# Kernel tuning notes

Hardware: AMD Instinct MI355X
Metric: run time of the kernel (lower is better)

Reference implementation:

```python
import jax, jax.numpy as jnp
import numpy as np

B, S, D, H = 2, 2048, 512, 8
HID = 512
DH = HID // H  # 64


def setup_inputs() -> dict:
    key = jax.random.key(0)
    ks = jax.random.split(key, 11)
    sc = 0.02
    return {
        "q": jax.random.normal(ks[0], (B, S, D), jnp.float32),
        "k": jax.random.normal(ks[1], (B, S, D), jnp.float32),
        "v": jax.random.normal(ks[2], (B, S, D), jnp.float32),
        "Wq": jax.random.normal(ks[3], (D, HID), jnp.float32) * sc,
        "bq": jnp.zeros((HID,), jnp.float32),
        "Wk": jax.random.normal(ks[4], (D, HID), jnp.float32) * sc,
        "bk": jnp.zeros((HID,), jnp.float32),
        "Wv": jax.random.normal(ks[5], (D, HID), jnp.float32) * sc,
        "bv": jnp.zeros((HID,), jnp.float32),
        "Wo": jax.random.normal(ks[6], (HID, D), jnp.float32) * sc,
        "bo": jnp.zeros((D,), jnp.float32),
    }


def reference(q, k, v, Wq, bq, Wk, bk, Wv, bv, Wo, bo):
    # Linear projections: [B,S,D] -> [B,S,HID]
    qp = q @ Wq + bq
    kp = k @ Wk + bk
    vp = v @ Wv + bv
    # Faithful to torch .view(B, -1, S, head_dim): raw reshape, NOT a
    # [B,S,H,d] transpose. Head i reads a contiguous block of the buffer.
    qh = qp.reshape(B, H, S, DH)
    kh = kp.reshape(B, H, S, DH)
    vh = vp.reshape(B, H, S, DH)
    # scores [B,H,S,S]; NOTE: original divides by sqrt(d) AFTER softmax.
    scores = jnp.einsum("bhsd,bhtd->bhst", qh, kh)
    attn = jax.nn.softmax(scores, axis=-1) / np.sqrt(DH).astype(np.float32)
    ctx = jnp.einsum("bhst,bhtd->bhsd", attn, vh)
    # torch.cat over heads along last dim -> [B,S,H*d] with head blocks
    concat = jnp.transpose(ctx, (0, 2, 1, 3)).reshape(B, S, HID)
    return concat @ Wo + bo
```

## Files before the change

### kernel.cpp

```cpp
#include <hip/hip_runtime.h>
#include <hip/hip_bf16.h>

typedef __bf16 bf16_t;
typedef __bf16 bf16x8 __attribute__((ext_vector_type(8)));
typedef __bf16 bf16x4 __attribute__((ext_vector_type(4)));
typedef short short4v __attribute__((ext_vector_type(4)));
typedef float f32x4 __attribute__((ext_vector_type(4)));

static_assert(sizeof(bf16x8) == 16, "bf16x8 must be 16B");

#define BB 2
#define SS 2048
#define DD 512
#define HH 8
#define DH 64
#define LOG2E 1.44269504088896f

__global__ void prep(const float* __restrict__ q, const float* __restrict__ k,
                     const float* __restrict__ v, const float* __restrict__ w0,
                     const float* __restrict__ w1, const float* __restrict__ w2,
                     const float* __restrict__ w3, bf16_t* __restrict__ qkvb,
                     bf16_t* __restrict__ wt, int n) {
  const int tid = threadIdx.x;
  if (blockIdx.z < 3) {
    const float* src = (blockIdx.z == 0) ? q : (blockIdx.z == 1) ? k : v;
    bf16_t* out = qkvb + (size_t)blockIdx.z * n;
    int i = (blockIdx.x * 256 + tid) * 8;
    if (i >= n) return;
    const float4* s4 = (const float4*)(src + i);
    float4 a = s4[0], b = s4[1];
    bf16x8 o;
    o[0] = (bf16_t)a.x; o[1] = (bf16_t)a.y; o[2] = (bf16_t)a.z; o[3] = (bf16_t)a.w;
    o[4] = (bf16_t)b.x; o[5] = (bf16_t)b.y; o[6] = (bf16_t)b.z; o[7] = (bf16_t)b.w;
    *(bf16x8*)(out + i) = o;
  } else {
    __shared__ float tile[32][33];
    const int x = blockIdx.x;
    const int wsel = x >> 8;
    const int nb = ((x >> 4) & 15) * 32, kb = (x & 15) * 32;
    const int tx = tid & 31, ty = tid >> 5;
    const float* W = (wsel == 0) ? w0 : (wsel == 1) ? w1 : (wsel == 2) ? w2 : w3;
    bf16_t* out = wt + (size_t)wsel * 512 * 512;
#pragma unroll
    for (int i = 0; i < 4; i++)
      tile[ty + i * 8][tx] = W[(size_t)(kb + ty + i * 8) * 512 + nb + tx];
    __syncthreads();
#pragma unroll
    for (int i = 0; i < 4; i++)
      out[(size_t)(nb + ty + i * 8) * 512 + kb + tx] = (bf16_t)tile[tx][ty + i * 8];
  }
}

template <int BM, int BN, int WM, int WN, typename OutT>
__global__ __launch_bounds__(256) void gemm2(
    const bf16_t* __restrict__ Abase, const bf16_t* __restrict__ Btbase,
    const float* __restrict__ bias0, const float* __restrict__ bias1,
    const float* __restrict__ bias2, OutT* __restrict__ Cbase,
    int M, int N, int K, long Az, long Bz, long Cz, float scale0) {
  static_assert(BM == 2 * WM && BN == 2 * WN, "2x2 wave grid");
  constexpr int FM = WM / 16, FN = WN / 16;
  constexpr int AJ = BM / 32, BJ = BN / 32;

  const bf16_t* A  = Abase + (size_t)blockIdx.z * Az;
  const bf16_t* Bt = Btbase + (size_t)blockIdx.z * Bz;
  const float* bias = (blockIdx.z == 0) ? bias0 : (blockIdx.z == 1) ? bias1 : bias2;
  OutT* C = Cbase + (size_t)blockIdx.z * Cz;
  const float osc = (blockIdx.z == 0) ? scale0 : 1.0f;

  __shared__ bf16_t As[2][BM * 64];
  __shared__ bf16_t Bs[2][BN * 64];

  const int tid = threadIdx.x, w = tid >> 6, l = tid & 63;
  const int bm = blockIdx.y, bn = blockIdx.x;
  const int wm0 = (w >> 1) * WM, wn0 = (w & 1) * WN;
  const int lr = l & 15, lg = l >> 4;

  f32x4 acc[FM][FN] = {};

  auto stage = [&](int buf, int kt) {
#pragma unroll
    for (int j = 0; j < AJ; j++) {
      int lin = j * 256 + tid;
      int row = lin >> 3, cc = lin & 7;
      const bf16_t* g = A + (size_t)(bm * BM + row) * K + kt * 64 + cc * 8;
      __builtin_amdgcn_global_load_lds(
          (const __attribute__((address_space(1))) void*)g,
          (__attribute__((address_space(3))) void*)(&As[buf][(j * 256 + w * 64) * 8]), 16, 0, 0);
    }
#pragma unroll
    for (int j = 0; j < BJ; j++) {
      int lin = j * 256 + tid;
      int row = lin >> 3, cc = lin & 7;
      const bf16_t* g = Bt + (size_t)(bn * BN + row) * K + kt * 64 + cc * 8;
      __builtin_amdgcn_global_load_lds(
          (const __attribute__((address_space(1))) void*)g,
          (__attribute__((address_space(3))) void*)(&Bs[buf][(j * 256 + w * 64) * 8]), 16, 0, 0);
    }
  };

  stage(0, 0);
  const int KT = K >> 6;
  for (int kt = 0; kt < KT; kt++) {
    __syncthreads();
    if (kt + 1 < KT) stage((kt + 1) & 1, kt + 1);
    const bf16_t* as = As[kt & 1];
    const bf16_t* bs = Bs[kt & 1];
#pragma unroll
    for (int kc = 0; kc < 2; kc++) {
      bf16x8 a[FM], b[FN];
#pragma unroll
      for (int i = 0; i < FM; i++)
        a[i] = *(const bf16x8*)(as + (wm0 + i * 16 + lr) * 64 + kc * 32 + lg * 8);
#pragma unroll
      for (int j = 0; j < FN; j++)
        b[j] = *(const bf16x8*)(bs + (wn0 + j * 16 + lr) * 64 + kc * 32 + lg * 8);
#pragma unroll
      for (int i = 0; i < FM; i++)
#pragma unroll
        for (int j = 0; j < FN; j++)
          acc[i][j] = __builtin_amdgcn_mfma_f32_16x16x32_bf16(a[i], b[j], acc[i][j], 0, 0, 0);
    }
  }

  const int row0 = bm * BM + wm0, col0 = bn * BN + wn0;
#pragma unroll
  for (int j = 0; j < FN; j++) {
    int col = col0 + j * 16 + lr;
    float bv = bias[col];
#pragma unroll
    for (int i = 0; i < FM; i++) {
      int row = row0 + i * 16 + lg * 4;
#pragma unroll
      for (int r = 0; r < 4; r++) {
        float vv = (acc[i][j][r] + bv) * osc;
        C[(size_t)(row + r) * N + col] = (OutT)vv;
      }
    }
  }
}

__global__ __launch_bounds__(256) void attn_flash(const bf16_t* __restrict__ qp,
                                                  const bf16_t* __restrict__ kp,
                                                  const bf16_t* __restrict__ vp,
                                                  float* __restrict__ Opart,
                                                  float* __restrict__ mlpart) {
  const int id = blockIdx.x;
  const int bh = (id & 7) | (((id >> 3) & 1) << 3);
  const int qt = (id >> 4) & 31;
  const int half = id >> 9;
  const int pidx = (((qt << 4) | bh) << 1) + half;

  const int tid = threadIdx.x, w = tid >> 6, l = tid & 63;
  const int lr = l & 15, lg = l >> 4;
  const size_t hb = (size_t)bh * (SS * DH);
  const bf16_t* Q = qp + hb;
  const bf16_t* Kh = kp + hb;
  const bf16_t* Vh = vp + hb;

  __shared__ __align__(16) bf16_t KsL[2][4096];
  __shared__ __align__(16) bf16_t VtL[2][4096];

  const int qr0 = qt * 64 + w * 16;

  bf16x8 aq[2];
#pragma unroll
  for (int kc = 0; kc < 2; kc++)
    aq[kc] = *(const bf16x8*)(Q + (size_t)(qr0 + lr) * DH + kc * 32 + lg * 8);

  f32x4 o[4] = {};
  float m_run = -1e30f, l_run = 0.f;

  const int krow = (w << 3) + (l >> 3);
  const int kcol = ((l & 7) ^ (l >> 3)) << 3;
  const bf16_t* ks_it = Kh + (size_t)(half * 16) * 4096 + krow * 64 + kcol;

  auto stage_k = [&](int buf, const bf16_t* ks) {
    char* kb = (char*)&KsL[buf][0];
    __builtin_amdgcn_global_load_lds((const __attribute__((address_space(1))) void*)ks,
        (__attribute__((address_space(3))) void*)(kb + (w << 10)), 16, 0, 0);
    __builtin_amdgcn_global_load_lds((const __attribute__((address_space(1))) void*)(ks + 2048),
        (__attribute__((address_space(3))) void*)(kb + 4096 + (w << 10)), 16, 0, 0);
  };

  const int vk0 = l, vd0 = w;
  const int vd1 = 4 + w;
  bf16x8 vreg0, vreg1;
  auto load_v = [&](int it) {
    const size_t kv0 = (size_t)it * 64;
    vreg0 = *(const bf16x8*)(Vh + (kv0 + vk0) * DH + vd0 * 8);
    vreg1 = *(const bf16x8*)(Vh + (kv0 + vk0) * DH + vd1 * 8);
  };
  auto write_v = [&](int buf) {
    char* vt = (char*)&VtL[buf][0];
#pragma unroll
    for (int j = 0; j < 8; j++) {
      int d0 = vd0 * 8 + j;
      *(bf16_t*)(vt + d0 * 128 + ((vk0 * 2) ^ (j << 4))) = vreg0[j];
    }
#pragma unroll
    for (int j = 0; j < 8; j++) {
      int d1 = vd1 * 8 + j;
      *(bf16_t*)(vt + d1 * 128 + ((vk0 * 2) ^ (j << 4))) = vreg1[j];
    }
  };

  const int it0 = half * 16;
  stage_k(0, ks_it);
  load_v(it0);
  write_v(0);

  f32x4 sA[4], sB[4];

#pragma unroll
  for (int T = 0; T <= 16; T++) {
    __syncthreads();

    if (T < 16) {
      f32x4* sc = (T & 1) ? sB : sA;
      const char* ksb = (const char*)&KsL[T & 1][0];
#pragma unroll
      for (int n = 0; n < 4; n++) sc[n] = f32x4{0.f, 0.f, 0.f, 0.f};
      __builtin_amdgcn_s_setprio(1);
#pragma unroll
      for (int kc = 0; kc < 2; kc++) {
#pragma unroll
        for (int n = 0; n < 4; n++) {
          bf16x8 bk = *(const bf16x8*)(ksb + (n * 16 + lr) * 128 +
                                       ((kc * 64 + lg * 16) ^ ((lr & 7) << 4)));
          sc[n] = __builtin_amdgcn_mfma_f32_16x16x32_bf16(bk, aq[kc], sc[n], 0, 0, 0);
        }
      }
      __builtin_amdgcn_s_setprio(0);
    }

    if (T + 1 < 16) {
      ks_it += 4096;
      stage_k((T + 1) & 1, ks_it);
      load_v(it0 + T + 1);
    }

    if (T >= 1) {
      f32x4* sp = (T & 1) ? sA : sB;

      float pmax = -1e30f;
#pragma unroll
      for (int n = 0; n < 4; n++)
#pragma unroll
        for (int r = 0; r < 4; r++) pmax = fmaxf(pmax, sp[n][r]);
      pmax = fmaxf(pmax, __shfl_xor(pmax, 16));
      pmax = fmaxf(pmax, __shfl_xor(pmax, 32));
      if (!__all(pmax <= m_run + 8.0f)) {
        float mnew = fmaxf(m_run, pmax);
        float scale = exp2f(m_run - mnew);
        l_run *= scale;
#pragma unroll
        for (int n = 0; n < 4; n++)
#pragma unroll
          for (int r = 0; r < 4; r++) o[n][r] *= scale;
        m_run = mnew;
      }
      float rs = 0.f;
#pragma unroll
      for (int n = 0; n < 4; n++)
#pragma unroll
        for (int r = 0; r < 4; r++) {
          float e = exp2f(sp[n][r] - m_run);
          sp[n][r] = e;
          rs += e;
        }
      l_run += rs;

      short4v pb[4];
#pragma unroll
      for (int c2 = 0; c2 < 4; c2++) {
        bf16x4 t;
#pragma unroll
        for (int r = 0; r < 4; r++) t[r] = (bf16_t)sp[c2][r];
        pb[c2] = __builtin_bit_cast(short4v, t);
      }
      const char* vtb = (const char*)&VtL[(T - 1) & 1][0];
      __builtin_amdgcn_s_setprio(1);
#pragma unroll
      for (int n = 0; n < 4; n++) {
#pragma unroll
        for (int c2 = 0; c2 < 4; c2++) {
          bf16x4 bvh = *(const bf16x4*)(vtb + (n * 16 + lr) * 128 +
                                        ((c2 * 32 + lg * 8) ^ ((lr & 7) << 4)));
          o[n] = __builtin_amdgcn_mfma_f32_16x16x16bf16_1k(
              __builtin_bit_cast(short4v, bvh), pb[c2], o[n], 0, 0, 0);
        }
      }
      __builtin_amdgcn_s_setprio(0);
    }

    __builtin_amdgcn_s_barrier();
    if (T + 1 < 16) write_v((T + 1) & 1);
  }

  l_run += __shfl_xor(l_run, 16);
  l_run += __shfl_xor(l_run, 32);

  float* ob = Opart + (size_t)pidx * 4096;
#pragma unroll
  for (int n = 0; n < 4; n++)
    *(f32x4*)(ob + ((w * 4 + n) * 64 + l) * 4) = o[n];
  if (lg == 0) {
    mlpart[(size_t)pidx * 128 + (w * 16 + lr) * 2 + 0] = m_run;
    mlpart[(size_t)pidx * 128 + (w * 16 + lr) * 2 + 1] = l_run;
  }
}

__global__ __launch_bounds__(256) void attn_combine(const float* __restrict__ Opart,
                                                    const float* __restrict__ mlpart,
                                                    bf16_t* __restrict__ ctx) {
  const int id = blockIdx.x;
  const int qt = id >> 4, bh = id & 15;
  const int t = threadIdx.x, w = t >> 6, l = t & 63;
  const int lr = l & 15, lg = l >> 4;
  const int p0 = id * 2, p1 = id * 2 + 1;
  const int q = w * 16 + lr;

  float m1 = mlpart[(size_t)p0 * 128 + q * 2 + 0];
  float l1 = mlpart[(size_t)p0 * 128 + q * 2 + 1];
  float m2 = mlpart[(size_t)p1 * 128 + q * 2 + 0];
  float l2 = mlpart[(size_t)p1 * 128 + q * 2 + 1];
  float m = fmaxf(m1, m2);
  float e1 = exp2f(m1 - m), e2 = exp2f(m2 - m);
  float denom = (l1 * e1 + l2 * e2) * 8.0f;
  float f1 = e1 / denom, f2 = e2 / denom;

  const int b = bh >> 3, h = bh & 7;
  const int trow = qt * 64 + q;
  size_t rowbase = ((size_t)b * SS + trow) * 512 + h * 64;

  const float* oa = Opart + (size_t)p0 * 4096;
  const float* obp = Opart + (size_t)p1 * 4096;
#pragma unroll
  for (int n = 0; n < 4; n++) {
    f32x4 a = *(const f32x4*)(oa + ((w * 4 + n) * 64 + l) * 4);
    f32x4 b2 = *(const f32x4*)(obp + ((w * 4 + n) * 64 + l) * 4);
    bf16x4 ov;
#pragma unroll
    for (int r = 0; r < 4; r++) ov[r] = (bf16_t)(a[r] * f1 + b2[r] * f2);
    *(bf16x4*)(&ctx[rowbase + n * 16 + lg * 4]) = ov;
  }
}

extern "C" void kernel_launch(void* const* d_in, const int* in_sizes, int n_in,
                              void* d_out, int out_size, void* d_ws, size_t ws_size,
                              hipStream_t stream) {
  const float* q  = (const float*)d_in[0];
  const float* k  = (const float*)d_in[1];
  const float* v  = (const float*)d_in[2];
  const float* Wq = (const float*)d_in[3];
  const float* bq = (const float*)d_in[4];
  const float* Wk = (const float*)d_in[5];
  const float* bk = (const float*)d_in[6];
  const float* Wv = (const float*)d_in[7];
  const float* bv = (const float*)d_in[8];
  const float* Wo = (const float*)d_in[9];
  const float* bo = (const float*)d_in[10];

  const size_t NQKV = (size_t)4096 * 512;
  const size_t NW = (size_t)512 * 512;

  bf16_t* ws   = (bf16_t*)d_ws;
  bf16_t* wt   = ws;
  bf16_t* proj = wt + 4 * NW;
  bf16_t* ctx  = proj + 3 * NQKV;
  bf16_t* qkvb = ctx + NQKV;
  float* Opart  = (float*)qkvb;
  float* mlpart = Opart + (size_t)1024 * 4096;

  prep<<<dim3(1024, 1, 4), 256, 0, stream>>>(q, k, v, Wq, Wk, Wv, Wo, qkvb, wt, (int)NQKV);
  gemm2<128, 64, 64, 32, bf16_t><<<dim3(8, 32, 3), 256, 0, stream>>>(
      qkvb, wt, bq, bk, bv, proj, 4096, 512, 512, (long)NQKV, (long)NW, (long)NQKV, LOG2E);
  attn_flash<<<1024, 256, 0, stream>>>(proj, proj + NQKV, proj + 2 * NQKV, Opart, mlpart);
  attn_combine<<<512, 256, 0, stream>>>(Opart, mlpart, ctx);
  gemm2<64, 64, 32, 32, float><<<dim3(8, 64, 1), 256, 0, stream>>>(
      ctx, wt + 3 * NW, bo, bo, bo, (float*)d_out, 4096, 512, 512, 0, 0, 0, 1.0f);
}
```

Before: 96.27 us.

## Split attention waves into 2x2 query/key quadrants with in-block softmax merge

Each wave now handles 32 query rows against half of the 64-key tile, instead of 16 query rows against the whole tile. Each K/V fragment loaded from LDS is reused across two query fragments, which halves LDS fragment reads per MFMA. The two key-half partial results are merged at the end through LDS before writing. The software-pipelined QK/softmax overlap is removed in favour of a simpler loop, and launch bounds now request 4 blocks per CU, which trades register budget for occupancy and adds an epilogue merge with extra barriers.

```diff
diff --git a/kernel.cpp b/kernel.cpp
--- a/kernel.cpp
+++ b/kernel.cpp
@@ -139,11 +139,11 @@
   }
 }
 
-__global__ __launch_bounds__(256) void attn_flash(const bf16_t* __restrict__ qp,
-                                                  const bf16_t* __restrict__ kp,
-                                                  const bf16_t* __restrict__ vp,
-                                                  float* __restrict__ Opart,
-                                                  float* __restrict__ mlpart) {
+__global__ __launch_bounds__(256, 4) void attn_flash(const bf16_t* __restrict__ qp,
+                                                     const bf16_t* __restrict__ kp,
+                                                     const bf16_t* __restrict__ vp,
+                                                     float* __restrict__ Opart,
+                                                     float* __restrict__ mlpart) {
   const int id = blockIdx.x;
   const int bh = (id & 7) | (((id >> 3) & 1) << 3);
   const int qt = (id >> 4) & 31;
@@ -152,6 +152,8 @@
 
   const int tid = threadIdx.x, w = tid >> 6, l = tid & 63;
   const int lr = l & 15, lg = l >> 4;
+  const int qh = w & 1;
+  const int kh = w >> 1;
   const size_t hb = (size_t)bh * (SS * DH);
   const bf16_t* Q = qp + hb;
   const bf16_t* Kh = kp + hb;
@@ -160,15 +162,17 @@
   __shared__ __align__(16) bf16_t KsL[2][4096];
   __shared__ __align__(16) bf16_t VtL[2][4096];
 
-  const int qr0 = qt * 64 + w * 16;
-
-  bf16x8 aq[2];
-#pragma unroll
-  for (int kc = 0; kc < 2; kc++)
-    aq[kc] = *(const bf16x8*)(Q + (size_t)(qr0 + lr) * DH + kc * 32 + lg * 8);
-
-  f32x4 o[4] = {};
-  float m_run = -1e30f, l_run = 0.f;
+  bf16x8 aq[2][2];
+#pragma unroll
+  for (int qf = 0; qf < 2; qf++)
+#pragma unroll
+    for (int kc = 0; kc < 2; kc++)
+      aq[qf][kc] = *(const bf16x8*)(Q + (size_t)(qt * 64 + qh * 32 + qf * 16 + lr) * DH +
+                                    kc * 32 + lg * 8);
+
+  f32x4 o[2][4] = {};
+  float m_run[2] = {-1e30f, -1e30f};
+  float l_run[2] = {0.f, 0.f};
 
   const int krow = (w << 3) + (l >> 3);
   const int kcol = ((l & 7) ^ (l >> 3)) << 3;
@@ -209,104 +213,143 @@
   load_v(it0);
   write_v(0);
 
-  f32x4 sA[4], sB[4];
-
-#pragma unroll
-  for (int T = 0; T <= 16; T++) {
+  for (int i = 0; i < 16; i++) {
+    const int buf = i & 1;
     __syncthreads();
-
-    if (T < 16) {
-      f32x4* sc = (T & 1) ? sB : sA;
-      const char* ksb = (const char*)&KsL[T & 1][0];
-#pragma unroll
-      for (int n = 0; n < 4; n++) sc[n] = f32x4{0.f, 0.f, 0.f, 0.f};
-      __builtin_amdgcn_s_setprio(1);
-#pragma unroll
-      for (int kc = 0; kc < 2; kc++) {
-#pragma unroll
-        for (int n = 0; n < 4; n++) {
-          bf16x8 bk = *(const bf16x8*)(ksb + (n * 16 + lr) * 128 +
-                                       ((kc * 64 + lg * 16) ^ ((lr & 7) << 4)));
-          sc[n] = __builtin_amdgcn_mfma_f32_16x16x32_bf16(bk, aq[kc], sc[n], 0, 0, 0);
-        }
-      }
-      __builtin_amdgcn_s_setprio(0);
-    }
-
-    if (T + 1 < 16) {
+    if (i + 1 < 16) {
       ks_it += 4096;
-      stage_k((T + 1) & 1, ks_it);
-      load_v(it0 + T + 1);
-    }
-
-    if (T >= 1) {
-      f32x4* sp = (T & 1) ? sA : sB;
-
+      stage_k(buf ^ 1, ks_it);
+      load_v(it0 + i + 1);
+    }
+
+    const char* ksb = (const char*)&KsL[buf][0];
+    f32x4 s[2][2] = {};
+    __builtin_amdgcn_s_setprio(1);
+#pragma unroll
+    for (int kc = 0; kc < 2; kc++) {
+#pragma unroll
+      for (int n = 0; n < 2; n++) {
+        bf16x8 bk = *(const bf16x8*)(ksb + (kh * 32 + n * 16 + lr) * 128 +
+                                     ((kc * 64 + lg * 16) ^ ((lr & 7) << 4)));
+#pragma unroll
+        for (int qf = 0; qf < 2; qf++)
+          s[qf][n] = __builtin_amdgcn_mfma_f32_16x16x32_bf16(bk, aq[qf][kc], s[qf][n], 0, 0, 0);
+      }
+    }
+    __builtin_amdgcn_s_setprio(0);
+
+#pragma unroll
+    for (int qf = 0; qf < 2; qf++) {
       float pmax = -1e30f;
 #pragma unroll
-      for (int n = 0; n < 4; n++)
-#pragma unroll
-        for (int r = 0; r < 4; r++) pmax = fmaxf(pmax, sp[n][r]);
+      for (int n = 0; n < 2; n++)
+#pragma unroll
+        for (int r = 0; r < 4; r++) pmax = fmaxf(pmax, s[qf][n][r]);
       pmax = fmaxf(pmax, __shfl_xor(pmax, 16));
       pmax = fmaxf(pmax, __shfl_xor(pmax, 32));
-      if (!__all(pmax <= m_run + 8.0f)) {
-        float mnew = fmaxf(m_run, pmax);
-        float scale = exp2f(m_run - mnew);
-        l_run *= scale;
+      if (!__all(pmax <= m_run[qf] + 8.0f)) {
+        float mnew = fmaxf(m_run[qf], pmax);
+        float scale = exp2f(m_run[qf] - mnew);
+        l_run[qf] *= scale;
 #pragma unroll
         for (int n = 0; n < 4; n++)
 #pragma unroll
-          for (int r = 0; r < 4; r++) o[n][r] *= scale;
-        m_run = mnew;
+          for (int r = 0; r < 4; r++) o[qf][n][r] *= scale;
+        m_run[qf] = mnew;
       }
       float rs = 0.f;
 #pragma unroll
-      for (int n = 0; n < 4; n++)
+      for (int n = 0; n < 2; n++)
 #pragma unroll
         for (int r = 0; r < 4; r++) {
-          float e = exp2f(sp[n][r] - m_run);
-          sp[n][r] = e;
+          float e = exp2f(s[qf][n][r] - m_run[qf]);
+          s[qf][n][r] = e;
           rs += e;
         }
-      l_run += rs;
-
-      short4v pb[4];
-#pragma unroll
-      for (int c2 = 0; c2 < 4; c2++) {
+      l_run[qf] += rs;
+    }
+
+    short4v pb[2][2];
+#pragma unroll
+    for (int qf = 0; qf < 2; qf++)
+#pragma unroll
+      for (int n = 0; n < 2; n++) {
         bf16x4 t;
 #pragma unroll
-        for (int r = 0; r < 4; r++) t[r] = (bf16_t)sp[c2][r];
-        pb[c2] = __builtin_bit_cast(short4v, t);
-      }
-      const char* vtb = (const char*)&VtL[(T - 1) & 1][0];
-      __builtin_amdgcn_s_setprio(1);
+        for (int r = 0; r < 4; r++) t[r] = (bf16_t)s[qf][n][r];
+        pb[qf][n] = __builtin_bit_cast(short4v, t);
+      }
+    const char* vtb = (const char*)&VtL[buf][0];
+    __builtin_amdgcn_s_setprio(1);
+#pragma unroll
+    for (int nd = 0; nd < 4; nd++) {
+#pragma unroll
+      for (int c2 = 0; c2 < 2; c2++) {
+        bf16x4 bvh = *(const bf16x4*)(vtb + (nd * 16 + lr) * 128 +
+                                      (((kh * 2 + c2) * 32 + lg * 8) ^ ((lr & 7) << 4)));
+#pragma unroll
+        for (int qf = 0; qf < 2; qf++)
+          o[qf][nd] = __builtin_amdgcn_mfma_f32_16x16x16bf16_1k(
+              __builtin_bit_cast(short4v, bvh), pb[qf][c2], o[qf][nd], 0, 0, 0);
+      }
+    }
+    __builtin_amdgcn_s_setprio(0);
+
+    if (i + 1 < 16) write_v(buf ^ 1);
+  }
+
+#pragma unroll
+  for (int qf = 0; qf < 2; qf++) {
+    l_run[qf] += __shfl_xor(l_run[qf], 16);
+    l_run[qf] += __shfl_xor(l_run[qf], 32);
+  }
+
+  __syncthreads();
+  float* scrO = (float*)&KsL[0][0];
+  float* scrM = (float*)&VtL[0][0];
+  if (w >= 2) {
+    float* po = scrO + (w - 2) * 2048;
+#pragma unroll
+    for (int qf = 0; qf < 2; qf++)
+#pragma unroll
+      for (int n = 0; n < 4; n++)
+        *(f32x4*)(po + ((qf * 4 + n) * 64 + l) * 4) = o[qf][n];
+    if (lg == 0) {
+      float* pm = scrM + (w - 2) * 256;
+#pragma unroll
+      for (int qf = 0; qf < 2; qf++) {
+        pm[qf * 32 + lr * 2 + 0] = m_run[qf];
+        pm[qf * 32 + lr * 2 + 1] = l_run[qf];
+      }
+    }
+  }
+  __syncthreads();
+  if (w < 2) {
+    float* po = scrO + w * 2048;
+    float* pm = scrM + w * 256;
+    float* ob = Opart + (size_t)pidx * 4096;
+#pragma unroll
+    for (int qf = 0; qf < 2; qf++) {
+      float mB = pm[qf * 32 + lr * 2 + 0];
+      float lB = pm[qf * 32 + lr * 2 + 1];
+      float mA = m_run[qf], lA = l_run[qf];
+      float mM = fmaxf(mA, mB);
+      float eA = exp2f(mA - mM), eB = exp2f(mB - mM);
+      float lM = lA * eA + lB * eB;
+      const int wg = w * 2 + qf;
 #pragma unroll
       for (int n = 0; n < 4; n++) {
-#pragma unroll
-        for (int c2 = 0; c2 < 4; c2++) {
-          bf16x4 bvh = *(const bf16x4*)(vtb + (n * 16 + lr) * 128 +
-                                        ((c2 * 32 + lg * 8) ^ ((lr & 7) << 4)));
-          o[n] = __builtin_amdgcn_mfma_f32_16x16x16bf16_1k(
-              __builtin_bit_cast(short4v, bvh), pb[c2], o[n], 0, 0, 0);
-        }
-      }
-      __builtin_amdgcn_s_setprio(0);
-    }
-
-    __builtin_amdgcn_s_barrier();
-    if (T + 1 < 16) write_v((T + 1) & 1);
-  }
-
-  l_run += __shfl_xor(l_run, 16);
-  l_run += __shfl_xor(l_run, 32);
-
-  float* ob = Opart + (size_t)pidx * 4096;
-#pragma unroll
-  for (int n = 0; n < 4; n++)
-    *(f32x4*)(ob + ((w * 4 + n) * 64 + l) * 4) = o[n];
-  if (lg == 0) {
-    mlpart[(size_t)pidx * 128 + (w * 16 + lr) * 2 + 0] = m_run;
-    mlpart[(size_t)pidx * 128 + (w * 16 + lr) * 2 + 1] = l_run;
+        f32x4 pv = *(const f32x4*)(po + ((qf * 4 + n) * 64 + l) * 4);
+        f32x4 om;
+#pragma unroll
+        for (int r = 0; r < 4; r++) om[r] = o[qf][n][r] * eA + pv[r] * eB;
+        *(f32x4*)(ob + ((wg * 4 + n) * 64 + l) * 4) = om;
+      }
+      if (lg == 0) {
+        mlpart[(size_t)pidx * 128 + (wg * 16 + lr) * 2 + 0] = mM;
+        mlpart[(size_t)pidx * 128 + (wg * 16 + lr) * 2 + 1] = lM;
+      }
+    }
   }
 }
 
```

After: 92.28 us. -4.1%, faster.
